# Performance work log

Measured on AMD Instinct MI355X. Metric: run time of the kernel, lower is better.

Reference implementation:

```python
import jax, jax.numpy as jnp
import numpy as np

DIM = 1024
HEADS = 16
DIM_HEAD = 64
INNER = HEADS * DIM_HEAD  # 1024
SCALE = DIM ** (-0.5)  # module scales by dim**-0.5 (not dim_head)


def setup_inputs() -> dict:
    key = jax.random.key(0)
    kx, kqkv, kwo, kbo = jax.random.split(key, 4)
    x = jax.random.normal(kx, (2, 2048, DIM), dtype=jnp.float32)
    W_qkv = jax.random.normal(kqkv, (DIM, 3 * INNER), dtype=jnp.float32) * (DIM ** -0.5)
    W_out = jax.random.normal(kwo, (INNER, DIM), dtype=jnp.float32) * (INNER ** -0.5)
    b_out = jax.random.normal(kbo, (DIM,), dtype=jnp.float32) * 0.01
    return {"x": x, "W_qkv": W_qkv, "W_out": W_out, "b_out": b_out}


def reference(x, W_qkv, W_out, b_out):
    b, n, _ = x.shape
    qkv = x @ W_qkv  # [b, n, 3*inner]
    q, k, v = jnp.split(qkv, 3, axis=-1)
    # [b, n, h*d] -> [b, h, n, d]
    reshape = lambda t: t.reshape(b, n, HEADS, DIM_HEAD).transpose(0, 2, 1, 3)
    q, k, v = reshape(q), reshape(k), reshape(v)
    dots = jnp.einsum('bhid,bhjd->bhij', q, k) * SCALE  # [b, h, n, n]
    attn = jax.nn.softmax(dots, axis=-1)
    out = jnp.einsum('bhij,bhjd->bhid', attn, v)  # [b, h, n, d]
    out = out.transpose(0, 2, 1, 3).reshape(b, n, INNER)
    return out @ W_out + b_out
```

## Files before the change

### kernel.cpp

```cpp
#include <hip/hip_runtime.h>

typedef __bf16 bf16x8 __attribute__((ext_vector_type(8)));
typedef __bf16 bf16x4 __attribute__((ext_vector_type(4)));
typedef float f32x4 __attribute__((ext_vector_type(4)));
typedef float f32x16 __attribute__((ext_vector_type(16)));

__device__ __forceinline__ void async16(void* lds, const void* g) {
  __builtin_amdgcn_global_load_lds(
      (__attribute__((address_space(1))) unsigned int*)(g),
      (__attribute__((address_space(3))) unsigned int*)(lds), 16, 0, 0);
}

__device__ __forceinline__ int detect_block(const unsigned short* win, int* cnt_sh) {
  if (threadIdx.x == 0) *cnt_sh = 0;
  __syncthreads();
  int c = 0;
#pragma unroll
  for (int j = 0; j < 8; j++) {
    const unsigned short u = win[threadIdx.x * 8 + j];
    if (((u >> 7) & 0xFF) >= 0xC0) c++;
  }
  if (c) atomicAdd(cnt_sh, c);
  __syncthreads();
  return (*cnt_sh >= 64) ? 1 : 0;
}

__global__ __launch_bounds__(256) void prep(
    const void* __restrict__ x, const void* __restrict__ Wqkv,
    const void* __restrict__ Wout, __bf16* __restrict__ xb,
    __bf16* __restrict__ WqkvT, __bf16* __restrict__ WoutT,
    int* __restrict__ flagp)
{
  __shared__ __bf16 tile[64 * 65];
  __shared__ int cnt;
  const int bx = blockIdx.x;
  const int t = threadIdx.x;

  if (bx < 2048) {
    const long base = (long)bx * 2048;
    const int f = detect_block((const unsigned short*)x + base, &cnt);
    if (bx == 0 && t == 0) *flagp = f;
    const long i = base + t * 8;
    if (f) {
      const float* s = (const float*)x;
#pragma unroll
      for (int j = 0; j < 8; j++) xb[i + j] = (__bf16)s[i + j];
    } else {
      *(bf16x8*)&xb[i] = *(const bf16x8*)((const __bf16*)x + i);
    }
    return;
  }

  const void* in;  __bf16* out;  int R = 1024, C, tcx, tr;
  if (bx < 2816) {
    const int idx = bx - 2048;
    in = Wqkv; out = WqkvT; C = 3072; tcx = (idx % 48) * 64; tr = (idx / 48) * 64;
  } else {
    const int idx = bx - 2816;
    in = Wout; out = WoutT; C = 1024; tcx = (idx % 16) * 64; tr = (idx / 16) * 64;
  }
  const int f = detect_block((const unsigned short*)in + (long)tr * C + tcx, &cnt);
#pragma unroll
  for (int i = 0; i < 16; i++) {
    const int idx = t + 256 * i;
    const int r = idx >> 6, c = idx & 63;
    const long g = (long)(tr + r) * C + tcx + c;
    tile[r * 65 + c] = f ? (__bf16)((const float*)in)[g] : ((const __bf16*)in)[g];
  }
  __syncthreads();
#pragma unroll
  for (int i = 0; i < 16; i++) {
    const int idx = t + 256 * i;
    const int r = idx >> 6, c = idx & 63;
    out[(long)(tcx + r) * R + tr + c] = tile[c * 65 + r];
  }
}

__global__ __launch_bounds__(256, 3) void gemm_qkv(
    const __bf16* __restrict__ A, const __bf16* __restrict__ Bt,
    __bf16* __restrict__ Cqk, __bf16* __restrict__ Vt)
{
  __shared__ __bf16 smem[17408];
  const int t = threadIdx.x;
  const int l = t & 63;
  const int w = t >> 6;
  const int wr = w >> 1, wc = w & 1;
  const long m0 = (long)blockIdx.x * 128;
  const long n0 = (long)blockIdx.y * 128;
  const int K = 1024;

  const int srow = w * 16 + (l >> 2);
  const int skof = (l & 3) * 8;
  const __bf16* gA = A + (m0 + srow) * (long)K + skof;
  const __bf16* gB = Bt + (n0 + srow) * (long)K + skof;
  const int Ao[2] = {0, 8192}, Bo[2] = {4096, 12288};
  const int lof = w * 512 + l * 8;

  async16(smem + Ao[0] + lof,        gA);
  async16(smem + Ao[0] + 2048 + lof, gA + 64 * (long)K);
  async16(smem + Bo[0] + lof,        gB);
  async16(smem + Bo[0] + 2048 + lof, gB + 64 * (long)K);
  gA += 32; gB += 32;
  __syncthreads();

  f32x4 acc[4][4] = {};

  for (int it = 0; it < 32; it++) {
    if (it < 31) {
      const int nb = (it + 1) & 1;
      async16(smem + Ao[nb] + lof,        gA);
      async16(smem + Ao[nb] + 2048 + lof, gA + 64 * (long)K);
      async16(smem + Bo[nb] + lof,        gB);
      async16(smem + Bo[nb] + 2048 + lof, gB + 64 * (long)K);
      gA += 32; gB += 32;
    }
    const __bf16* As = smem + Ao[it & 1];
    const __bf16* Bs = smem + Bo[it & 1];
    bf16x8 af[4], bfr[4];
#pragma unroll
    for (int mi = 0; mi < 4; mi++)
      af[mi] = *(const bf16x8*)&As[(wr * 64 + mi * 16 + (l & 15)) * 32 + (l >> 4) * 8];
#pragma unroll
    for (int ni = 0; ni < 4; ni++)
      bfr[ni] = *(const bf16x8*)&Bs[(wc * 64 + ni * 16 + (l & 15)) * 32 + (l >> 4) * 8];
#pragma unroll
    for (int mi = 0; mi < 4; mi++)
#pragma unroll
      for (int ni = 0; ni < 4; ni++)
        acc[mi][ni] = __builtin_amdgcn_mfma_f32_16x16x32_bf16(af[mi], bfr[ni], acc[mi][ni], 0, 0, 0);
    __syncthreads();
  }

  if (n0 < 2048) {
#pragma unroll
    for (int mi = 0; mi < 4; mi++)
#pragma unroll
      for (int ni = 0; ni < 4; ni++) {
        const long col = n0 + wc * 64 + ni * 16 + (l & 15);
#pragma unroll
        for (int r = 0; r < 4; r++) {
          const long row = m0 + wr * 64 + mi * 16 + (l >> 4) * 4 + r;
          Cqk[row * 2048 + col] = (__bf16)acc[mi][ni][r];
        }
      }
  } else {
#pragma unroll
    for (int mi = 0; mi < 4; mi++)
#pragma unroll
      for (int ni = 0; ni < 4; ni++) {
        const int c = wc * 64 + ni * 16 + (l & 15);
        const int r = wr * 64 + mi * 16 + (l >> 4) * 4;
        bf16x4 pk;
#pragma unroll
        for (int k = 0; k < 4; k++) pk[k] = (__bf16)acc[mi][ni][k];
        *(bf16x4*)&smem[c * 136 + r] = pk;
      }
    __syncthreads();
    const int b = (int)(m0 >> 11);
    const int nbase = (int)(m0 & 2047);
#pragma unroll
    for (int i = 0; i < 8; i++) {
      const int c = (t >> 4) + i * 16;
      const int r8 = (t & 15) * 8;
      const bf16x8 v = *(const bf16x8*)&smem[c * 136 + r8];
      const int vcol = (int)(n0 - 2048) + c;
      *(bf16x8*)&Vt[((long)(b * 16 + (vcol >> 6)) * 64 + (vcol & 63)) * 2048 + nbase + r8] = v;
    }
  }
}

__global__ __launch_bounds__(256, 2) void gemm_out(
    const __bf16* __restrict__ A, const __bf16* __restrict__ Bt,
    const void* __restrict__ bias_raw, void* __restrict__ C,
    const int* __restrict__ flagp)
{
  __shared__ __bf16 smem[12288];
  const int t = threadIdx.x;
  const int l = t & 63;
  const int w = t >> 6;
  const int wr = w >> 1, wc = w & 1;
  const long m0 = (long)blockIdx.x * 128;
  const long n0 = (long)blockIdx.y * 64;
  const int of = *flagp;
  const int K = 1024;

  const int srow = w * 16 + (l >> 2);
  const int skof = (l & 3) * 8;
  const __bf16* gA = A + (m0 + srow) * (long)K + skof;
  const __bf16* gB = Bt + (n0 + srow) * (long)K + skof;
  const int Ao[2] = {0, 6144}, Bo[2] = {4096, 10240};
  const int lof = w * 512 + l * 8;

  async16(smem + Ao[0] + lof,        gA);
  async16(smem + Ao[0] + 2048 + lof, gA + 64 * (long)K);
  async16(smem + Bo[0] + lof,        gB);
  gA += 32; gB += 32;
  __syncthreads();

  f32x4 acc[4][2] = {};

  for (int it = 0; it < 32; it++) {
    if (it < 31) {
      const int nb = (it + 1) & 1;
      async16(smem + Ao[nb] + lof,        gA);
      async16(smem + Ao[nb] + 2048 + lof, gA + 64 * (long)K);
      async16(smem + Bo[nb] + lof,        gB);
      gA += 32; gB += 32;
    }
    const __bf16* As = smem + Ao[it & 1];
    const __bf16* Bs = smem + Bo[it & 1];
    bf16x8 af[4], bfr[2];
#pragma unroll
    for (int mi = 0; mi < 4; mi++)
      af[mi] = *(const bf16x8*)&As[(wr * 64 + mi * 16 + (l & 15)) * 32 + (l >> 4) * 8];
#pragma unroll
    for (int ni = 0; ni < 2; ni++)
      bfr[ni] = *(const bf16x8*)&Bs[(wc * 32 + ni * 16 + (l & 15)) * 32 + (l >> 4) * 8];
#pragma unroll
    for (int mi = 0; mi < 4; mi++)
#pragma unroll
      for (int ni = 0; ni < 2; ni++)
        acc[mi][ni] = __builtin_amdgcn_mfma_f32_16x16x32_bf16(af[mi], bfr[ni], acc[mi][ni], 0, 0, 0);
    __syncthreads();
  }

#pragma unroll
  for (int mi = 0; mi < 4; mi++)
#pragma unroll
    for (int ni = 0; ni < 2; ni++) {
      const long col = n0 + wc * 32 + ni * 16 + (l & 15);
      const float bv = of ? ((const float*)bias_raw)[col]
                          : (float)((const __bf16*)bias_raw)[col];
#pragma unroll
      for (int r = 0; r < 4; r++) {
        const long row = m0 + wr * 64 + mi * 16 + (l >> 4) * 4 + r;
        const float val = acc[mi][ni][r] + bv;
        const long off = row * 1024 + col;
        if (of) ((float*)C)[off] = val;
        else    ((__bf16*)C)[off] = (__bf16)val;
      }
    }
}

#define EXP2_SCALE 0.045084439f

__global__ __launch_bounds__(256, 4) void attn_kernel(
    const __bf16* __restrict__ qk, const __bf16* __restrict__ Vt,
    __bf16* __restrict__ O)
{
  __shared__ __bf16 smem[20480];
  const int t = threadIdx.x;
  const int l = t & 63;
  const int w = t >> 6;
  const int wi = w & 1, wj = w >> 1;
  const int hl = l >> 5;
  const int i7 = l & 7;
  const int L = blockIdx.y * 32 + blockIdx.x;
  const int bh = (L & 7) * 4 + ((L >> 3) & 3);
  const int qt = L >> 5;
  const int b = bh >> 4, head = bh & 15;
  const long q_row0 = (long)b * 2048 + qt * 64;

  const int srow = w * 8 + (l >> 3);
  const int sdof = ((l & 7) ^ (l >> 3)) * 8;
  const int lof = w * 512 + l * 8;
  const int Ko[2] = {4096, 12288}, Vo[2] = {8192, 16384};

  {
    const __bf16* g = qk + (q_row0 + srow) * 2048 + head * 64 + sdof;
    async16(smem + lof,        g);
    async16(smem + 2048 + lof, g + (long)32 * 2048);
  }
  const __bf16* gK = qk + ((long)b * 2048 + srow) * 2048 + 1024 + head * 64 + sdof;
  const __bf16* gV = Vt + ((long)bh * 64 + srow) * 2048 + sdof;
  async16(smem + Ko[0] + lof,        gK);
  async16(smem + Ko[0] + 2048 + lof, gK + 32 * 2048);
  async16(smem + Vo[0] + lof,        gV);
  async16(smem + Vo[0] + 2048 + lof, gV + 32 * 2048);
  gK += (long)64 * 2048;
  gV += 64;
  __syncthreads();

  bf16x8 qf[4];
#pragma unroll
  for (int kc = 0; kc < 4; kc++)
    qf[kc] = *(const bf16x8*)&smem[(wi * 32 + (l & 31)) * 64 + (((kc * 2 + hl) ^ i7) * 8)];

  __bf16* Ps = smem;
  f32x16 acc = {0,0,0,0,0,0,0,0,0,0,0,0,0,0,0,0};
  float l_i = 0.0f;

  for (int it = 0; it < 32; it++) {
    __syncthreads();
    const __bf16* Ks = smem + Ko[it & 1];
    const __bf16* Vs = smem + Vo[it & 1];

    f32x16 st = {0,0,0,0,0,0,0,0,0,0,0,0,0,0,0,0};
#pragma unroll
    for (int kc = 0; kc < 4; kc++) {
      const bf16x8 ak = *(const bf16x8*)&Ks[(wj * 32 + (l & 31)) * 64 + (((kc * 2 + hl) ^ i7) * 8)];
      st = __builtin_amdgcn_mfma_f32_32x32x16_bf16(ak, qf[kc], st, 0, 0, 0);
    }

    float rs = 0.0f;
#pragma unroll
    for (int r = 0; r < 16; r++) {
      const float p = exp2f(st[r] * EXP2_SCALE);
      st[r] = p;
      rs += p;
    }
    rs += __shfl_xor(rs, 32, 64);
    l_i += rs;

    {
      const int ibase = (wi * 32 + (l & 31)) * 64;
      const int sub = 4 * hl;
#pragma unroll
      for (int q = 0; q < 4; q++) {
        bf16x4 pk;
#pragma unroll
        for (int r = 0; r < 4; r++) pk[r] = (__bf16)st[q * 4 + r];
        const int gj = 4 * wj + q;
        *(bf16x4*)&Ps[ibase + ((gj ^ i7) * 8) + sub] = pk;
      }
    }
    __syncthreads();

    if (it < 31) {
      const int nb = (it + 1) & 1;
      async16(smem + Ko[nb] + lof,        gK);
      async16(smem + Ko[nb] + 2048 + lof, gK + 32 * 2048);
      async16(smem + Vo[nb] + lof,        gV);
      async16(smem + Vo[nb] + 2048 + lof, gV + 32 * 2048);
      gK += (long)64 * 2048;
      gV += 64;
    }

#pragma unroll
    for (int kc = 0; kc < 4; kc++) {
      const int swz = ((kc * 2 + hl) ^ i7) * 8;
      const bf16x8 ap = *(const bf16x8*)&Ps[(wi * 32 + (l & 31)) * 64 + swz];
      const bf16x8 bv = *(const bf16x8*)&Vs[(wj * 32 + (l & 31)) * 64 + swz];
      acc = __builtin_amdgcn_mfma_f32_32x32x16_bf16(ap, bv, acc, 0, 0, 0);
    }
  }

  __syncthreads();
  float* lb = (float*)(smem + 12288);
  if (l < 32) lb[w * 32 + l] = l_i;
  __syncthreads();
#pragma unroll
  for (int r = 0; r < 16; r++) {
    const int iloc = (r & 3) + 8 * (r >> 2) + 4 * hl;
    const float lt = lb[wi * 32 + iloc] + lb[(wi + 2) * 32 + iloc];
    const long row = q_row0 + wi * 32 + iloc;
    const long col = (long)head * 64 + wj * 32 + (l & 31);
    O[row * 1024 + col] = (__bf16)(acc[r] / lt);
  }
}

extern "C" void kernel_launch(void* const* d_in, const int* in_sizes, int n_in,
                              void* d_out, int out_size, void* d_ws, size_t ws_size,
                              hipStream_t stream) {
  const void* x    = d_in[0];
  const void* Wqkv = d_in[1];
  const void* Wout = d_in[2];
  const void* bout = d_in[3];

  char* ws = (char*)d_ws;
  int*    flagp = (int*)ws;
  __bf16* xb    = (__bf16*)(ws + 4096);
  __bf16* Obuf  = xb;
  __bf16* WqkvT = (__bf16*)(ws + 4096 +  8388608);
  __bf16* WoutT = (__bf16*)(ws + 4096 + 14680064);
  __bf16* qkbuf = (__bf16*)(ws + 4096 + 16777216);
  __bf16* VtBuf = (__bf16*)(ws + 4096 + 33554432);

  hipLaunchKernelGGL(prep, dim3(3072), dim3(256), 0, stream,
                     x, Wqkv, Wout, xb, WqkvT, WoutT, flagp);
  hipLaunchKernelGGL(gemm_qkv, dim3(32, 24), dim3(256), 0, stream,
                     xb, WqkvT, qkbuf, VtBuf);
  hipLaunchKernelGGL(attn_kernel, dim3(32, 32), dim3(256), 0, stream,
                     qkbuf, VtBuf, Obuf);
  hipLaunchKernelGGL(gemm_out, dim3(32, 16), dim3(256), 0, stream,
                     Obuf, WoutT, bout, d_out, flagp);
}
```

Measured before the change: 206.4 us.

## Keep P in registers via permlane32 swap and split PV across key halves

The attention kernel no longer writes the softmax probabilities P to shared memory. It repacks the MFMA S-tile outputs into PV A-operands with v_permlane32_swap, so each wave multiplies its own key half by V for all 64 output columns. The partial outputs from the two key-half waves are then reduced through LDS at the end. This removes one __syncthreads and the P store/load per iteration, moves the next K/V prefetch to the top of the loop, loads Q straight from global into registers, shrinks LDS, and adds s_setprio around MFMA blocks. In exchange there are more accumulator registers (two f32x16) and an extra end-of-kernel reduction, which could hurt occupancy.

```diff
diff --git a/kernel.cpp b/kernel.cpp
--- a/kernel.cpp
+++ b/kernel.cpp
@@ -2,13 +2,33 @@
 
 typedef __bf16 bf16x8 __attribute__((ext_vector_type(8)));
 typedef __bf16 bf16x4 __attribute__((ext_vector_type(4)));
+typedef __bf16 bf16x2 __attribute__((ext_vector_type(2)));
 typedef float f32x4 __attribute__((ext_vector_type(4)));
 typedef float f32x16 __attribute__((ext_vector_type(16)));
+typedef int i32x4 __attribute__((ext_vector_type(4)));
+typedef unsigned int u32x2 __attribute__((ext_vector_type(2)));
 
 __device__ __forceinline__ void async16(void* lds, const void* g) {
   __builtin_amdgcn_global_load_lds(
       (__attribute__((address_space(1))) unsigned int*)(g),
       (__attribute__((address_space(3))) unsigned int*)(lds), 16, 0, 0);
+}
+
+__device__ __forceinline__ unsigned int pack2(float a, float b) {
+  bf16x2 t;
+  t[0] = (__bf16)a;
+  t[1] = (__bf16)b;
+  return __builtin_bit_cast(unsigned int, t);
+}
+
+__device__ __forceinline__ void plswap(unsigned int& d, unsigned int& s) {
+#if __has_builtin(__builtin_amdgcn_permlane32_swap)
+  u32x2 r = __builtin_amdgcn_permlane32_swap(d, s, false, false);
+  d = r[0];
+  s = r[1];
+#else
+  asm("v_permlane32_swap_b32 %0, %1" : "+v"(d), "+v"(s));
+#endif
 }
 
 __device__ __forceinline__ int detect_block(const unsigned short* win, int* cnt_sh) {
@@ -248,7 +268,7 @@
     const __bf16* __restrict__ qk, const __bf16* __restrict__ Vt,
     __bf16* __restrict__ O)
 {
-  __shared__ __bf16 smem[20480];
+  __shared__ __bf16 smem[16384];
   const int t = threadIdx.x;
   const int l = t & 63;
   const int w = t >> 6;
@@ -264,43 +284,50 @@
   const int srow = w * 8 + (l >> 3);
   const int sdof = ((l & 7) ^ (l >> 3)) * 8;
   const int lof = w * 512 + l * 8;
-  const int Ko[2] = {4096, 12288}, Vo[2] = {8192, 16384};
-
-  {
-    const __bf16* g = qk + (q_row0 + srow) * 2048 + head * 64 + sdof;
-    async16(smem + lof,        g);
-    async16(smem + 2048 + lof, g + (long)32 * 2048);
-  }
+
   const __bf16* gK = qk + ((long)b * 2048 + srow) * 2048 + 1024 + head * 64 + sdof;
   const __bf16* gV = Vt + ((long)bh * 64 + srow) * 2048 + sdof;
-  async16(smem + Ko[0] + lof,        gK);
-  async16(smem + Ko[0] + 2048 + lof, gK + 32 * 2048);
-  async16(smem + Vo[0] + lof,        gV);
-  async16(smem + Vo[0] + 2048 + lof, gV + 32 * 2048);
+  async16(smem + lof,        gK);
+  async16(smem + 2048 + lof, gK + 32 * 2048);
+  async16(smem + 4096 + lof, gV);
+  async16(smem + 6144 + lof, gV + 32 * 2048);
   gK += (long)64 * 2048;
   gV += 64;
-  __syncthreads();
 
   bf16x8 qf[4];
-#pragma unroll
-  for (int kc = 0; kc < 4; kc++)
-    qf[kc] = *(const bf16x8*)&smem[(wi * 32 + (l & 31)) * 64 + (((kc * 2 + hl) ^ i7) * 8)];
-
-  __bf16* Ps = smem;
-  f32x16 acc = {0,0,0,0,0,0,0,0,0,0,0,0,0,0,0,0};
+  {
+    const __bf16* gQ = qk + (q_row0 + wi * 32 + (l & 31)) * 2048 + head * 64 + hl * 8;
+#pragma unroll
+    for (int kc = 0; kc < 4; kc++)
+      qf[kc] = *(const bf16x8*)(gQ + kc * 16);
+  }
+
+  f32x16 accA = {0,0,0,0,0,0,0,0,0,0,0,0,0,0,0,0};
+  f32x16 accB = {0,0,0,0,0,0,0,0,0,0,0,0,0,0,0,0};
   float l_i = 0.0f;
 
   for (int it = 0; it < 32; it++) {
     __syncthreads();
-    const __bf16* Ks = smem + Ko[it & 1];
-    const __bf16* Vs = smem + Vo[it & 1];
+    if (it < 31) {
+      const int nb = ((it + 1) & 1) * 8192;
+      async16(smem + nb + lof,        gK);
+      async16(smem + nb + 2048 + lof, gK + 32 * 2048);
+      async16(smem + nb + 4096 + lof, gV);
+      async16(smem + nb + 6144 + lof, gV + 32 * 2048);
+      gK += (long)64 * 2048;
+      gV += 64;
+    }
+    const __bf16* Ks = smem + (it & 1) * 8192;
+    const __bf16* Vs = Ks + 4096;
 
     f32x16 st = {0,0,0,0,0,0,0,0,0,0,0,0,0,0,0,0};
+    __builtin_amdgcn_s_setprio(1);
 #pragma unroll
     for (int kc = 0; kc < 4; kc++) {
       const bf16x8 ak = *(const bf16x8*)&Ks[(wj * 32 + (l & 31)) * 64 + (((kc * 2 + hl) ^ i7) * 8)];
       st = __builtin_amdgcn_mfma_f32_32x32x16_bf16(ak, qf[kc], st, 0, 0, 0);
     }
+    __builtin_amdgcn_s_setprio(0);
 
     float rs = 0.0f;
 #pragma unroll
@@ -312,50 +339,50 @@
     rs += __shfl_xor(rs, 32, 64);
     l_i += rs;
 
-    {
-      const int ibase = (wi * 32 + (l & 31)) * 64;
-      const int sub = 4 * hl;
-#pragma unroll
-      for (int q = 0; q < 4; q++) {
-        bf16x4 pk;
-#pragma unroll
-        for (int r = 0; r < 4; r++) pk[r] = (__bf16)st[q * 4 + r];
-        const int gj = 4 * wj + q;
-        *(bf16x4*)&Ps[ibase + ((gj ^ i7) * 8) + sub] = pk;
-      }
-    }
-    __syncthreads();
-
-    if (it < 31) {
-      const int nb = (it + 1) & 1;
-      async16(smem + Ko[nb] + lof,        gK);
-      async16(smem + Ko[nb] + 2048 + lof, gK + 32 * 2048);
-      async16(smem + Vo[nb] + lof,        gV);
-      async16(smem + Vo[nb] + 2048 + lof, gV + 32 * 2048);
-      gK += (long)64 * 2048;
-      gV += 64;
-    }
-
-#pragma unroll
-    for (int kc = 0; kc < 4; kc++) {
-      const int swz = ((kc * 2 + hl) ^ i7) * 8;
-      const bf16x8 ap = *(const bf16x8*)&Ps[(wi * 32 + (l & 31)) * 64 + swz];
-      const bf16x8 bv = *(const bf16x8*)&Vs[(wj * 32 + (l & 31)) * 64 + swz];
-      acc = __builtin_amdgcn_mfma_f32_32x32x16_bf16(ap, bv, acc, 0, 0, 0);
-    }
-  }
-
-  __syncthreads();
-  float* lb = (float*)(smem + 12288);
+    unsigned int a0 = pack2(st[0],  st[1]),  b0 = pack2(st[4],  st[5]);
+    unsigned int c0 = pack2(st[2],  st[3]),  d0 = pack2(st[6],  st[7]);
+    unsigned int a1 = pack2(st[8],  st[9]),  b1 = pack2(st[12], st[13]);
+    unsigned int c1 = pack2(st[10], st[11]), d1 = pack2(st[14], st[15]);
+    plswap(a0, b0);
+    plswap(c0, d0);
+    plswap(a1, b1);
+    plswap(c1, d1);
+    const i32x4 f0 = {(int)a0, (int)c0, (int)b0, (int)d0};
+    const i32x4 f1 = {(int)a1, (int)c1, (int)b1, (int)d1};
+    const bf16x8 pa0 = __builtin_bit_cast(bf16x8, f0);
+    const bf16x8 pa1 = __builtin_bit_cast(bf16x8, f1);
+
+    const int vg = wj * 4;
+    const bf16x8 bv00 = *(const bf16x8*)&Vs[((l & 31)) * 64      + (((vg + hl) ^ i7) * 8)];
+    const bf16x8 bv01 = *(const bf16x8*)&Vs[(32 + (l & 31)) * 64 + (((vg + hl) ^ i7) * 8)];
+    const bf16x8 bv10 = *(const bf16x8*)&Vs[((l & 31)) * 64      + (((vg + 2 + hl) ^ i7) * 8)];
+    const bf16x8 bv11 = *(const bf16x8*)&Vs[(32 + (l & 31)) * 64 + (((vg + 2 + hl) ^ i7) * 8)];
+    __builtin_amdgcn_s_setprio(1);
+    accA = __builtin_amdgcn_mfma_f32_32x32x16_bf16(pa0, bv00, accA, 0, 0, 0);
+    accB = __builtin_amdgcn_mfma_f32_32x32x16_bf16(pa0, bv01, accB, 0, 0, 0);
+    accA = __builtin_amdgcn_mfma_f32_32x32x16_bf16(pa1, bv10, accA, 0, 0, 0);
+    accB = __builtin_amdgcn_mfma_f32_32x32x16_bf16(pa1, bv11, accB, 0, 0, 0);
+    __builtin_amdgcn_s_setprio(0);
+  }
+
+  __syncthreads();
+  float* xbf = (float*)smem;
+  float* lb  = (float*)(smem + 8192);
+#pragma unroll
+  for (int r = 0; r < 16; r++)
+    xbf[w * 1024 + r * 64 + l] = wj ? accA[r] : accB[r];
   if (l < 32) lb[w * 32 + l] = l_i;
   __syncthreads();
+  const int pw = 2 * (1 - wj) + wi;
 #pragma unroll
   for (int r = 0; r < 16; r++) {
     const int iloc = (r & 3) + 8 * (r >> 2) + 4 * hl;
     const float lt = lb[wi * 32 + iloc] + lb[(wi + 2) * 32 + iloc];
+    const float own = wj ? accB[r] : accA[r];
+    const float o = own + xbf[pw * 1024 + r * 64 + l];
     const long row = q_row0 + wi * 32 + iloc;
     const long col = (long)head * 64 + wj * 32 + (l & 31);
-    O[row * 1024 + col] = (__bf16)(acc[r] / lt);
+    O[row * 1024 + col] = (__bf16)(o / lt);
   }
 }
 
```

Result: faster. 200.2 us (-3.0%).
